# Kernel tuning notes

Measured on AMD Instinct MI355X. Metric: run time of the kernel, lower is better.

Reference implementation:

```python
import jax, jax.numpy as jnp
import numpy as np

N, E = 50000, 800000
NODE_IN, EDGE_IN, H, L = 2, 2, 128, 3
EPS = 1e-5


def _lin(x, W, b):
    return x @ W + b


def setup_inputs() -> dict:
    key = jax.random.key(0)
    ks = jax.random.split(key, 24)

    def gw(k, shape):
        fan_in = shape[-2]
        return jax.random.uniform(k, shape, jnp.float32, -1.0, 1.0) / np.sqrt(fan_in)

    inp = {
        "x": jax.random.normal(ks[0], (N, NODE_IN), jnp.float32),
        "edge_attr": jax.random.normal(ks[1], (E, EDGE_IN), jnp.float32),
        "edge_index": jax.random.randint(ks[2], (2, E), 0, N, jnp.int32),
        "batch": jnp.zeros((N,), jnp.int32),
        # input MLP: [NODE_IN -> H -> H], Lin+ReLU twice
        "Win0": gw(ks[3], (NODE_IN, H)), "bin0": jnp.zeros((H,), jnp.float32),
        "Win1": gw(ks[4], (H, H)), "bin1": jnp.zeros((H,), jnp.float32),
        # per-layer (stacked over L) IGConv params
        # mlp1: [H+EDGE_IN -> H -> H], Lin+ReLU twice
        "W1a": gw(ks[5], (L, H + EDGE_IN, H)), "b1a": jnp.zeros((L, H), jnp.float32),
        "W1b": gw(ks[6], (L, H, H)), "b1b": jnp.zeros((L, H), jnp.float32),
        # mlp2: [2H -> H] Lin+ReLU, then Lin+Sigmoid [H -> H]
        "W2a": gw(ks[7], (L, 2 * H, H)), "b2a": jnp.zeros((L, H), jnp.float32),
        "W2b": gw(ks[8], (L, H, H)), "b2b": jnp.zeros((L, H), jnp.float32),
        # BatchNorm affine params per layer
        "gamma": jnp.ones((L, H), jnp.float32), "beta": jnp.zeros((L, H), jnp.float32),
        # final MLP: [H -> H] Lin+ReLU, then Lin+Sigmoid [H -> 1]
        "Wf": gw(ks[9], (H, H)), "bf": jnp.zeros((H,), jnp.float32),
        "Wo": gw(ks[10], (H, 1)), "bo": jnp.zeros((1,), jnp.float32),
    }
    return inp


def _forward(x, edge_attr, edge_index, Win0, bin0, Win1, bin1,
             W1a, b1a, W1b, b1b, W2a, b2a, W2b, b2b, gamma, beta, Wf, bf, Wo, bo):
    src, dst = edge_index[0], edge_index[1]  # PyG source->target flow
    n = x.shape[0]

    # input MLP
    h = jax.nn.relu(_lin(x, Win0, bin0))
    h = jax.nn.relu(_lin(h, Win1, bin1))

    # per-edge mean-aggregation denominator (0-degree nodes -> 0 in PyG mean)
    cnt = jax.ops.segment_sum(jnp.ones((src.shape[0],), h.dtype), dst, num_segments=n)
    denom = jnp.maximum(cnt, 1.0)[:, None]  # [N,1]

    for l in range(L):
        # message: mlp1(cat(x_j, edge_attr))
        xj = h[src]                                        # [E,H] gather
        tmp = jnp.concatenate([xj, edge_attr], axis=1)     # [E,H+EDGE_IN]
        m = jax.nn.relu(_lin(tmp, W1a[l], b1a[l]))
        m = jax.nn.relu(_lin(m, W1b[l], b1b[l]))           # [E,H]
        # mean aggregate at targets
        agg = jax.ops.segment_sum(m, dst, num_segments=n) / denom  # [N,H]
        # update: mlp2(cat(x, agg)) -> Lin+ReLU -> Lin+Sigmoid
        u = jnp.concatenate([h, agg], axis=1)
        u = jax.nn.relu(_lin(u, W2a[l], b2a[l]))
        out = jax.nn.sigmoid(_lin(u, W2b[l], b2b[l]))
        # residual + BatchNorm (training-mode batch stats, biased var)
        r = h + out
        mu = jnp.mean(r, axis=0)
        var = jnp.mean((r - mu) ** 2, axis=0)
        h = (r - mu) * jax.lax.rsqrt(var + EPS) * gamma[l] + beta[l]

    # final MLP
    f = jax.nn.relu(_lin(h, Wf, bf))
    return jax.nn.sigmoid(_lin(f, Wo, bo))  # [N,1]


def reference(x, edge_attr, edge_index, batch, Win0, bin0, Win1, bin1,
              W1a, b1a, W1b, b1b, W2a, b2a, W2b, b2b, gamma, beta, Wf, bf, Wo, bo):
    # `batch` is unused by the original forward
    return _forward(x, edge_attr, edge_index, Win0, bin0, Win1, bin1,
                    W1a, b1a, W1b, b1b, W2a, b2a, W2b, b2b, gamma, beta,
                    Wf, bf, Wo, bo)
```

## Files before the change

### kernel.cpp

```cpp
#include <hip/hip_runtime.h>
#include <hip/hip_bf16.h>

#define NN 50000
#define NE 800000
#define HD 128
#define EPSV 1e-5f
#define TE 64
#define BLK 256
#define SROW 68
#define ASTR 336
#define BSTR 272

typedef unsigned short u16;
typedef __attribute__((ext_vector_type(8))) short bf16x8;
typedef __attribute__((ext_vector_type(4))) float f32x4;
#define MFMA16 __builtin_amdgcn_mfma_f32_16x16x32_bf16

__device__ __forceinline__ float sigm(float x){ return 1.0f/(1.0f+__expf(-x)); }
__device__ __forceinline__ void atomAddF(float* p, float v){ unsafeAtomicAdd(p, v); }
__device__ __forceinline__ unsigned bfr(float x){
    unsigned u = __float_as_uint(x);
    return (u + 0x7FFFu + ((u>>16)&1u)) >> 16;
}
__device__ __forceinline__ float bf2f(unsigned u){ return __uint_as_float(u<<16); }

__global__ void zero_i_k(int* __restrict__ p, int n){
    int i = blockIdx.x*blockDim.x + threadIdx.x;
    if (i < n) p[i] = 0;
}

__global__ void zero_agg_bn_k(float4* __restrict__ agg4, int n4, float* __restrict__ bn){
    int i = blockIdx.x*blockDim.x + threadIdx.x;
    if (i < n4) agg4[i] = make_float4(0.f,0.f,0.f,0.f);
    if (i < 256) bn[i] = 0.0f;
}

__global__ void count_k(const int* __restrict__ dst, int* __restrict__ cnt){
    int e = blockIdx.x*blockDim.x + threadIdx.x;
    if (e < NE) atomicAdd(&cnt[dst[e]], 1);
}
__global__ void rdenom_k(const int* __restrict__ cnt, float* __restrict__ rd){
    int i = blockIdx.x*blockDim.x + threadIdx.x;
    if (i < NN) rd[i] = 1.0f / fmaxf((float)cnt[i], 1.0f);
}

__global__ __launch_bounds__(1024) void scan_k(const int* __restrict__ cnt, int* __restrict__ off){
    __shared__ int s[1024];
    __shared__ int carryS;
    const int tid = threadIdx.x;
    if (tid == 0) carryS = 0;
    __syncthreads();
    const int NCH = (NN + 1023) / 1024;
    for (int ch = 0; ch < NCH; ++ch){
        const int i = ch*1024 + tid;
        const int v = (i < NN) ? cnt[i] : 0;
        s[tid] = v;
        __syncthreads();
        #pragma unroll
        for (int ofs = 1; ofs < 1024; ofs <<= 1){
            int t = (tid >= ofs) ? s[tid-ofs] : 0;
            __syncthreads();
            s[tid] += t;
            __syncthreads();
        }
        const int carry = carryS;
        if (i < NN) off[i] = carry + s[tid] - v;
        __syncthreads();
        if (tid == 1023) carryS = carry + s[1023];
        __syncthreads();
    }
    if (tid == 0) off[NN] = NE;
}

__global__ void fill_k(const int* __restrict__ src, const int* __restrict__ dst,
                       const float* __restrict__ ea, const int* __restrict__ off,
                       int* __restrict__ fill, int* __restrict__ ssrc,
                       unsigned* __restrict__ sea, int* __restrict__ sdst){
    int e = blockIdx.x*blockDim.x + threadIdx.x;
    if (e < NE){
        int d = dst[e];
        int pos = atomicAdd(&fill[d], 1);
        int slot = off[d] + pos;
        ssrc[slot] = src[e];
        sdst[slot] = d;
        const float2 a = *(const float2*)&ea[(size_t)e*2];
        sea[slot] = bfr(a.x) | (bfr(a.y)<<16);
    }
}

__global__ void wconv_k(const float* __restrict__ src, u16* __restrict__ dst,
                        int K, int KP, int H){
    int idx = blockIdx.x*blockDim.x + threadIdx.x;
    if (idx >= H*KP) return;
    const int l = blockIdx.y;
    src += (size_t)l*K*H;  dst += (size_t)l*H*KP;
    int c = idx / KP, k = idx - c*KP;
    dst[idx] = (k < K) ? (u16)bfr(src[k*H + c]) : (u16)0;
}

__device__ __forceinline__ void mv_acc(const float* sT, int krows,
        const float* __restrict__ W, int c0, int eg, float acc[4][8])
{
    const float* Wp = W + c0;
    #pragma unroll 2
    for (int k=0; k<krows; ++k) {
        const float4 sv = *(const float4*)(sT + k*SROW + eg*4);
        const float4 wa = *(const float4*)(Wp + k*HD);
        const float4 wb = *(const float4*)(Wp + k*HD + 4);
        const float s[4] = {sv.x, sv.y, sv.z, sv.w};
        const float w[8] = {wa.x,wa.y,wa.z,wa.w, wb.x,wb.y,wb.z,wb.w};
        #pragma unroll
        for (int i=0;i<4;++i)
            #pragma unroll
            for (int j=0;j<8;++j)
                acc[i][j] = fmaf(s[i], w[j], acc[i][j]);
    }
}

__device__ __forceinline__ void stage_rows(float* smem, const float* __restrict__ base,
                                           const int* rowsLDS, int tid)
{
    const int e_lo = tid>>3, kq = tid&7;
    #pragma unroll
    for (int half=0; half<2; ++half) {
        const int e = e_lo + 32*half;
        const int row = rowsLDS[e];
        const float* p = base + (size_t)row*HD + kq*4;
        #pragma unroll
        for (int q=0; q<4; ++q) {
            const float4 v = *(const float4*)(p + q*32);
            const int kb = 4*kq + 32*q;
            smem[(kb+0)*SROW + e] = v.x;
            smem[(kb+1)*SROW + e] = v.y;
            smem[(kb+2)*SROW + e] = v.z;
            smem[(kb+3)*SROW + e] = v.w;
        }
    }
}

__global__ __launch_bounds__(BLK) void input_mlp_k(
    const float* __restrict__ x,
    const float* __restrict__ W0, const float* __restrict__ b0,
    const float* __restrict__ W1, const float* __restrict__ b1,
    float* __restrict__ h, u16* __restrict__ hb)
{
    __shared__ float smem[130*SROW];
    const int tid = threadIdx.x;
    const int n0 = blockIdx.x * TE;

    #pragma unroll
    for (int it=0; it<(HD*TE)/BLK; ++it) {
        int task = it*BLK + tid;
        int e = task & (TE-1);
        int c = task >> 6;
        int n = n0 + e; if (n >= NN) n = NN-1;
        float x0 = x[n*2+0], x1 = x[n*2+1];
        smem[c*SROW + e] = fmaxf(fmaf(x0, W0[c], fmaf(x1, W0[HD+c], b0[c])), 0.0f);
    }
    __syncthreads();

    const int cg = tid & 15, eg = tid >> 4, c0 = cg*8;
    float acc[4][8];
    #pragma unroll
    for (int j=0;j<8;++j){ float bv=b1[c0+j];
        #pragma unroll
        for (int i=0;i<4;++i) acc[i][j]=bv; }
    mv_acc(smem, HD, W1, c0, eg, acc);

    #pragma unroll
    for (int i=0;i<4;++i){
        int n = n0 + eg*4 + i;
        if (n < NN) {
            float4 r0, r1;
            r0.x=fmaxf(acc[i][0],0.f); r0.y=fmaxf(acc[i][1],0.f);
            r0.z=fmaxf(acc[i][2],0.f); r0.w=fmaxf(acc[i][3],0.f);
            r1.x=fmaxf(acc[i][4],0.f); r1.y=fmaxf(acc[i][5],0.f);
            r1.z=fmaxf(acc[i][6],0.f); r1.w=fmaxf(acc[i][7],0.f);
            *(float4*)&h[(size_t)n*HD + c0]     = r0;
            *(float4*)&h[(size_t)n*HD + c0 + 4] = r1;
            uint4 pk;
            pk.x = bfr(r0.x)|(bfr(r0.y)<<16); pk.y = bfr(r0.z)|(bfr(r0.w)<<16);
            pk.z = bfr(r1.x)|(bfr(r1.y)<<16); pk.w = bfr(r1.z)|(bfr(r1.w)<<16);
            *(uint4*)&hb[(size_t)n*HD + c0] = pk;
        }
    }
}

__global__ __launch_bounds__(BLK, 7) void edge_msg_kernel(
    const u16* __restrict__ hb,
    const int* __restrict__ ssrc, const unsigned* __restrict__ sea,
    const int* __restrict__ sdst, const int* __restrict__ off,
    const float* __restrict__ rd,
    const u16* __restrict__ W1aT, const float* __restrict__ b1a,
    const u16* __restrict__ W1bT, const float* __restrict__ b1b,
    float* __restrict__ agg)
{
    __shared__ char bufA[TE*ASTR];

    const int tid = threadIdx.x;
    const int lane = tid & 63;
    const int l15 = lane & 15, lhi = lane >> 4;
    const int w = tid >> 6;
    const int s0 = blockIdx.x * TE;
    const int cg = tid & 15, c0 = cg*8;
    const int myrow = tid >> 2, p = tid & 3;
    const int rowL = 16*w + l15;
    const int bl = lane >> 2;

    const int d0 = sdst[s0];
    const int d1 = sdst[s0 + TE - 1];

    for (int idx = tid; idx < TE*4; idx += BLK){
        const int r = idx >> 2, q = idx & 3;
        *(uint4*)(bufA + r*ASTR + 272 + q*16) = make_uint4(0u,0u,0u,0u);
    }

    {
        const int sv0 = ssrc[s0 + rowL];
        const int sv  = __shfl(sv0, bl);
        const uint4* sp = (const uint4*)(hb + (size_t)sv*HD);
        uint4* dp = (uint4*)(bufA + myrow*ASTR + p*64);
        #pragma unroll
        for (int q=0;q<4;++q) dp[q] = sp[p*4+q];
        if (p == 0){
            const unsigned eaw = sea[s0 + myrow];
            *(uint4*)(bufA + myrow*ASTR + 256) = make_uint4(eaw, 0u, 0u, 0u);
        }
    }
    __syncthreads();

    f32x4 acc1[2][4];
    #pragma unroll
    for (int cc=0; cc<2; ++cc){
        const float4 bv = *(const float4*)&b1a[(2*w+cc)*16 + lhi*4];
        #pragma unroll
        for (int te=0; te<4; ++te){
            acc1[cc][te][0]=bv.x; acc1[cc][te][1]=bv.y;
            acc1[cc][te][2]=bv.z; acc1[cc][te][3]=bv.w;
        }
    }
    #pragma unroll
    for (int kk=0; kk<5; ++kk){
        const bf16x8 a0 = *(const bf16x8*)(W1aT + ((2*w  )*16 + l15)*160 + kk*32 + lhi*8);
        const bf16x8 a1 = *(const bf16x8*)(W1aT + ((2*w+1)*16 + l15)*160 + kk*32 + lhi*8);
        #pragma unroll
        for (int te=0; te<4; ++te){
            const bf16x8 bb = *(const bf16x8*)(bufA + (te*16+l15)*ASTR + kk*64 + lhi*16);
            acc1[0][te] = MFMA16(a0, bb, acc1[0][te], 0,0,0);
            acc1[1][te] = MFMA16(a1, bb, acc1[1][te], 0,0,0);
        }
    }
    __syncthreads();
    #pragma unroll
    for (int cc=0; cc<2; ++cc){
        #pragma unroll
        for (int te=0; te<4; ++te){
            uint2 pk;
            pk.x = bfr(fmaxf(acc1[cc][te][0],0.f)) | (bfr(fmaxf(acc1[cc][te][1],0.f))<<16);
            pk.y = bfr(fmaxf(acc1[cc][te][2],0.f)) | (bfr(fmaxf(acc1[cc][te][3],0.f))<<16);
            *(uint2*)(bufA + (te*16+l15)*ASTR + (2*w+cc)*32 + lhi*8) = pk;
        }
    }
    __syncthreads();

    f32x4 acc2[2][4];
    #pragma unroll
    for (int cc=0; cc<2; ++cc){
        const float4 bv = *(const float4*)&b1b[(2*w+cc)*16 + lhi*4];
        #pragma unroll
        for (int te=0; te<4; ++te){
            acc2[cc][te][0]=bv.x; acc2[cc][te][1]=bv.y;
            acc2[cc][te][2]=bv.z; acc2[cc][te][3]=bv.w;
        }
    }
    #pragma unroll
    for (int kk=0; kk<4; ++kk){
        const bf16x8 a0 = *(const bf16x8*)(W1bT + ((2*w  )*16 + l15)*128 + kk*32 + lhi*8);
        const bf16x8 a1 = *(const bf16x8*)(W1bT + ((2*w+1)*16 + l15)*128 + kk*32 + lhi*8);
        #pragma unroll
        for (int te=0; te<4; ++te){
            const bf16x8 bb = *(const bf16x8*)(bufA + (te*16+l15)*ASTR + kk*64 + lhi*16);
            acc2[0][te] = MFMA16(a0, bb, acc2[0][te], 0,0,0);
            acc2[1][te] = MFMA16(a1, bb, acc2[1][te], 0,0,0);
        }
    }
    __syncthreads();
    #pragma unroll
    for (int cc=0; cc<2; ++cc){
        #pragma unroll
        for (int te=0; te<4; ++te){
            uint2 pk;
            pk.x = bfr(fmaxf(acc2[cc][te][0],0.f)) | (bfr(fmaxf(acc2[cc][te][1],0.f))<<16);
            pk.y = bfr(fmaxf(acc2[cc][te][2],0.f)) | (bfr(fmaxf(acc2[cc][te][3],0.f))<<16);
            *(uint2*)(bufA + (te*16+l15)*ASTR + (2*w+cc)*32 + lhi*8) = pk;
        }
    }
    __syncthreads();

    const int ng = tid >> 4;
    for (int d = d0 + ng; d <= d1; d += 16){
        const int ob = off[d], oe = off[d+1];
        int lo = ob > s0 ? ob : s0;
        int hi = oe < s0 + TE ? oe : s0 + TE;
        if (lo >= hi) continue;
        float s[8] = {0.f,0.f,0.f,0.f,0.f,0.f,0.f,0.f};
        for (int t = lo; t < hi; ++t){
            const uint4 v = *(const uint4*)(bufA + (t - s0)*ASTR + cg*16);
            s[0] += bf2f(v.x&0xffffu); s[1] += bf2f(v.x>>16);
            s[2] += bf2f(v.y&0xffffu); s[3] += bf2f(v.y>>16);
            s[4] += bf2f(v.z&0xffffu); s[5] += bf2f(v.z>>16);
            s[6] += bf2f(v.w&0xffffu); s[7] += bf2f(v.w>>16);
        }
        const float rdv = rd[d];
        #pragma unroll
        for (int j=0;j<8;++j) s[j] *= rdv;
        float* ap = &agg[(size_t)d*HD + c0];
        if (ob >= s0 && oe <= s0 + TE){
            float4 a0 = make_float4(s[0],s[1],s[2],s[3]);
            float4 a1 = make_float4(s[4],s[5],s[6],s[7]);
            *(float4*)ap = a0; *(float4*)(ap+4) = a1;
        } else {
            #pragma unroll
            for (int j=0;j<8;++j) atomAddF(ap+j, s[j]);
        }
    }
}

__global__ __launch_bounds__(BLK, 4) void node_upd_kernel(
    const float* __restrict__ h, const u16* __restrict__ hb,
    const float* __restrict__ agg,
    const u16* __restrict__ W2aT, const float* __restrict__ b2a,
    const u16* __restrict__ W2bT, const float* __restrict__ b2b,
    float* __restrict__ rbuf)
{
    __shared__ char bufA[TE*ASTR];
    __shared__ char bufB[TE*BSTR];

    const int tid = threadIdx.x;
    const int lane = tid & 63;
    const int l15 = lane & 15, lhi = lane >> 4;
    const int w = tid >> 6;
    const int n0 = blockIdx.x * TE;
    const int myrow = tid >> 2, p = tid & 3;

    {
        int n = n0 + myrow; if (n >= NN) n = NN-1;
        const uint4* sp = (const uint4*)(hb + (size_t)n*HD);
        uint4* dp = (uint4*)(bufA + myrow*ASTR + p*64);
        #pragma unroll
        for (int q=0;q<4;++q) dp[q] = sp[p*4+q];
    }
    __syncthreads();

    f32x4 accN[2][4];
    #pragma unroll
    for (int cc=0; cc<2; ++cc){
        const float4 bv = *(const float4*)&b2a[(2*w+cc)*16 + lhi*4];
        #pragma unroll
        for (int te=0; te<4; ++te){
            accN[cc][te][0]=bv.x; accN[cc][te][1]=bv.y;
            accN[cc][te][2]=bv.z; accN[cc][te][3]=bv.w;
        }
    }
    #pragma unroll
    for (int kk=0; kk<4; ++kk){
        const bf16x8 a0 = *(const bf16x8*)(W2aT + ((2*w  )*16 + l15)*256 + kk*32 + lhi*8);
        const bf16x8 a1 = *(const bf16x8*)(W2aT + ((2*w+1)*16 + l15)*256 + kk*32 + lhi*8);
        #pragma unroll
        for (int te=0; te<4; ++te){
            const bf16x8 bb = *(const bf16x8*)(bufA + (te*16+l15)*ASTR + kk*64 + lhi*16);
            accN[0][te] = MFMA16(a0, bb, accN[0][te], 0,0,0);
            accN[1][te] = MFMA16(a1, bb, accN[1][te], 0,0,0);
        }
    }
    __syncthreads();
    {
        int n = n0 + myrow; if (n >= NN) n = NN-1;
        const float4* sp = (const float4*)(agg + (size_t)n*HD + p*32);
        uint4* dp = (uint4*)(bufA + myrow*ASTR + p*64);
        #pragma unroll
        for (int q=0;q<4;++q){
            const float4 v0 = sp[q*2+0], v1 = sp[q*2+1];
            uint4 pk;
            pk.x = bfr(v0.x)|(bfr(v0.y)<<16); pk.y = bfr(v0.z)|(bfr(v0.w)<<16);
            pk.z = bfr(v1.x)|(bfr(v1.y)<<16); pk.w = bfr(v1.z)|(bfr(v1.w)<<16);
            dp[q] = pk;
        }
    }
    __syncthreads();
    #pragma unroll
    for (int kk=0; kk<4; ++kk){
        const bf16x8 a0 = *(const bf16x8*)(W2aT + ((2*w  )*16 + l15)*256 + 128 + kk*32 + lhi*8);
        const bf16x8 a1 = *(const bf16x8*)(W2aT + ((2*w+1)*16 + l15)*256 + 128 + kk*32 + lhi*8);
        #pragma unroll
        for (int te=0; te<4; ++te){
            const bf16x8 bb = *(const bf16x8*)(bufA + (te*16+l15)*ASTR + kk*64 + lhi*16);
            accN[0][te] = MFMA16(a0, bb, accN[0][te], 0,0,0);
            accN[1][te] = MFMA16(a1, bb, accN[1][te], 0,0,0);
        }
    }
    #pragma unroll
    for (int cc=0; cc<2; ++cc){
        #pragma unroll
        for (int te=0; te<4; ++te){
            uint2 pk;
            pk.x = bfr(fmaxf(accN[cc][te][0],0.f)) | (bfr(fmaxf(accN[cc][te][1],0.f))<<16);
            pk.y = bfr(fmaxf(accN[cc][te][2],0.f)) | (bfr(fmaxf(accN[cc][te][3],0.f))<<16);
            *(uint2*)(bufB + (te*16+l15)*BSTR + (2*w+cc)*32 + lhi*8) = pk;
        }
    }
    __syncthreads();

    f32x4 accO[2][4];
    #pragma unroll
    for (int cc=0; cc<2; ++cc){
        const float4 bv = *(const float4*)&b2b[(2*w+cc)*16 + lhi*4];
        #pragma unroll
        for (int te=0; te<4; ++te){
            accO[cc][te][0]=bv.x; accO[cc][te][1]=bv.y;
            accO[cc][te][2]=bv.z; accO[cc][te][3]=bv.w;
        }
    }
    #pragma unroll
    for (int kk=0; kk<4; ++kk){
        const bf16x8 a0 = *(const bf16x8*)(W2bT + ((2*w  )*16 + l15)*128 + kk*32 + lhi*8);
        const bf16x8 a1 = *(const bf16x8*)(W2bT + ((2*w+1)*16 + l15)*128 + kk*32 + lhi*8);
        #pragma unroll
        for (int te=0; te<4; ++te){
            const bf16x8 bb = *(const bf16x8*)(bufB + (te*16+l15)*BSTR + kk*64 + lhi*16);
            accO[0][te] = MFMA16(a0, bb, accO[0][te], 0,0,0);
            accO[1][te] = MFMA16(a1, bb, accO[1][te], 0,0,0);
        }
    }
    #pragma unroll
    for (int cc=0; cc<2; ++cc){
        const int cbase = (2*w+cc)*16 + lhi*4;
        #pragma unroll
        for (int te=0; te<4; ++te){
            const int n = n0 + te*16 + l15;
            if (n < NN){
                const float4 hv = *(const float4*)&h[(size_t)n*HD + cbase];
                float4 r;
                r.x = hv.x + sigm(accO[cc][te][0]);
                r.y = hv.y + sigm(accO[cc][te][1]);
                r.z = hv.z + sigm(accO[cc][te][2]);
                r.w = hv.w + sigm(accO[cc][te][3]);
                *(float4*)&rbuf[(size_t)n*HD + cbase] = r;
            }
        }
    }
}

__global__ void bn_stats_k(const float* __restrict__ r, float* __restrict__ bn){
    const int c = threadIdx.x & (HD-1);
    const int half = threadIdx.x >> 7;
    const int stride = gridDim.x * 2;
    float s = 0.f, ss = 0.f;
    for (int n = blockIdx.x*2 + half; n < NN; n += stride) {
        const float v = r[(size_t)n*HD + c];
        s += v; ss += v*v;
    }
    atomAddF(&bn[c], s);
    atomAddF(&bn[HD+c], ss);
}

__global__ void bn_norm_k(const float* __restrict__ r, const float* __restrict__ bn,
                          const float* __restrict__ gamma, const float* __restrict__ beta,
                          float* __restrict__ h, u16* __restrict__ hb){
    const int i = blockIdx.x*blockDim.x + threadIdx.x;
    const int n4 = NN*HD/4;
    if (i >= n4) return;
    const int c0 = (i*4) & (HD-1);
    float4 v = ((const float4*)r)[i];
    float* vp = (float*)&v;
    #pragma unroll
    for (int j=0;j<4;++j){
        const int c = c0 + j;
        const float mu  = bn[c] * (1.0f/NN);
        const float var = bn[HD+c] * (1.0f/NN) - mu*mu;
        const float sc  = rsqrtf(var + EPSV) * gamma[c];
        const float sh  = beta[c] - mu*sc;
        vp[j] = fmaf(vp[j], sc, sh);
    }
    ((float4*)h)[i] = v;
    uint2 pk;
    pk.x = bfr(vp[0]) | (bfr(vp[1])<<16);
    pk.y = bfr(vp[2]) | (bfr(vp[3])<<16);
    ((uint2*)hb)[i] = pk;
}

__global__ __launch_bounds__(BLK) void final_kernel(
    const float* __restrict__ h,
    const float* __restrict__ Wf, const float* __restrict__ bf,
    const float* __restrict__ Wo, const float* __restrict__ bo,
    float* __restrict__ out)
{
    __shared__ float smem[130*SROW];
    __shared__ int s_src[TE];
    const int tid = threadIdx.x;
    const int n0 = blockIdx.x * TE;
    const int cg = tid & 15, eg = tid >> 4, c0 = cg*8;

    if (tid < TE) { int n = n0 + tid; s_src[tid] = (n < NN) ? n : NN-1; }
    __syncthreads();
    stage_rows(smem, h, s_src, tid);
    __syncthreads();

    float acc[4][8];
    #pragma unroll
    for (int j=0;j<8;++j){ float bv=bf[c0+j];
        #pragma unroll
        for (int i=0;i<4;++i) acc[i][j]=bv; }
    mv_acc(smem, HD, Wf, c0, eg, acc);
    __syncthreads();

    #pragma unroll
    for (int j=0;j<8;++j){
        float4 m0;
        m0.x=fmaxf(acc[0][j],0.f); m0.y=fmaxf(acc[1][j],0.f);
        m0.z=fmaxf(acc[2][j],0.f); m0.w=fmaxf(acc[3][j],0.f);
        *(float4*)&smem[(c0+j)*SROW + eg*4] = m0;
    }
    __syncthreads();

    const int e = tid >> 2, q = tid & 3;
    float s = 0.f;
    #pragma unroll
    for (int kk=0; kk<32; ++kk) {
        const int k = q*32 + kk;
        s = fmaf(smem[k*SROW + e], Wo[k], s);
    }
    s += __shfl_xor(s, 1);
    s += __shfl_xor(s, 2);
    const int n = n0 + e;
    if (q == 0 && n < NN)
        out[n] = sigm(s + bo[0]);
}

extern "C" void kernel_launch(void* const* d_in, const int* in_sizes, int n_in,
                              void* d_out, int out_size, void* d_ws, size_t ws_size,
                              hipStream_t stream)
{
    const float* x    = (const float*)d_in[0];
    const float* ea   = (const float*)d_in[1];
    const int*   ei   = (const int*)d_in[2];
    const float* Win0 = (const float*)d_in[4];
    const float* bin0 = (const float*)d_in[5];
    const float* Win1 = (const float*)d_in[6];
    const float* bin1 = (const float*)d_in[7];
    const float* W1a  = (const float*)d_in[8];
    const float* b1a  = (const float*)d_in[9];
    const float* W1b  = (const float*)d_in[10];
    const float* b1b  = (const float*)d_in[11];
    const float* W2a  = (const float*)d_in[12];
    const float* b2a  = (const float*)d_in[13];
    const float* W2b  = (const float*)d_in[14];
    const float* b2b  = (const float*)d_in[15];
    const float* gmm  = (const float*)d_in[16];
    const float* bta  = (const float*)d_in[17];
    const float* Wf   = (const float*)d_in[18];
    const float* bfv  = (const float*)d_in[19];
    const float* Wo   = (const float*)d_in[20];
    const float* bo   = (const float*)d_in[21];
    float* out = (float*)d_out;

    char* p = (char*)d_ws;
    float* h     = (float*)p;  p += (size_t)NN*HD*4;
    float* rbuf  = (float*)p;  p += (size_t)NN*HD*4;
    float* agg   = (float*)p;  p += (size_t)NN*HD*4;
    u16*   hb    = (u16*)p;    p += (size_t)NN*HD*2;
    u16*   W1aT  = (u16*)p;    p += (size_t)3*128*160*2;
    u16*   W1bT  = (u16*)p;    p += (size_t)3*128*128*2;
    u16*   W2aT  = (u16*)p;    p += (size_t)3*128*256*2;
    u16*   W2bT  = (u16*)p;    p += (size_t)3*128*128*2;
    float* rd    = (float*)p;  p += (size_t)NN*4;
    float* bn    = (float*)p;  p += 256*4;
    int*   cnt   = (int*)p;    p += (size_t)NN*4;
    int*   fill  = (int*)p;    p += (size_t)NN*4;
    int*   off   = (int*)p;    p += (size_t)(NN+1)*4;
    int*   ssrc  = (int*)p;    p += (size_t)NE*4;
    int*   sdst  = (int*)p;    p += (size_t)NE*4;
    unsigned* sea = (unsigned*)p;

    const int* srcp = ei;
    const int* dstp = ei + NE;

    const int GN = (NN + TE - 1) / TE;
    const int GE = NE / TE;
    const int G4 = (NN*HD/4 + 255) / 256;

    zero_i_k<<<(2*NN+255)/256, 256, 0, stream>>>(cnt, 2*NN);
    count_k<<<(NE+255)/256, 256, 0, stream>>>(dstp, cnt);
    scan_k<<<1, 1024, 0, stream>>>(cnt, off);
    rdenom_k<<<(NN+255)/256, 256, 0, stream>>>(cnt, rd);
    fill_k<<<(NE+255)/256, 256, 0, stream>>>(srcp, dstp, ea, off, fill, ssrc, sea, sdst);

    wconv_k<<<dim3((128*160+255)/256,3), 256, 0, stream>>>(W1a, W1aT, 130, 160, 128);
    wconv_k<<<dim3((128*128+255)/256,3), 256, 0, stream>>>(W1b, W1bT, 128, 128, 128);
    wconv_k<<<dim3((128*256+255)/256,3), 256, 0, stream>>>(W2a, W2aT, 256, 256, 128);
    wconv_k<<<dim3((128*128+255)/256,3), 256, 0, stream>>>(W2b, W2bT, 128, 128, 128);

    input_mlp_k<<<GN, BLK, 0, stream>>>(x, Win0, bin0, Win1, bin1, h, hb);

    for (int l = 0; l < 3; ++l) {
        zero_agg_bn_k<<<G4, 256, 0, stream>>>((float4*)agg, NN*HD/4, bn);
        edge_msg_kernel<<<GE, BLK, 0, stream>>>(hb, ssrc, sea, sdst, off, rd,
            W1aT + (size_t)l*128*160, b1a + l*HD,
            W1bT + (size_t)l*128*128, b1b + l*HD, agg);
        node_upd_kernel<<<GN, BLK, 0, stream>>>(h, hb, agg,
            W2aT + (size_t)l*128*256, b2a + l*HD,
            W2bT + (size_t)l*128*128, b2b + l*HD, rbuf);
        bn_stats_k<<<400, 256, 0, stream>>>(rbuf, bn);
        bn_norm_k<<<G4, 256, 0, stream>>>(rbuf, bn, gmm + l*HD, bta + l*HD, h, hb);
    }

    final_kernel<<<GN, BLK, 0, stream>>>(h, Wf, bfv, Wo, bo, out);
}
```

Baseline: 1.048 ms.

## Fuse BN stats into node update, parallelize scan, fold agg zeroing into BN

Replaces the single-block serial prefix scan with a three-kernel parallel block scan. Computes BatchNorm sum and sum-of-squares inside the node update epilogue with wave shuffles and atomics, which removes a separate full read of rbuf per layer. Zeroing of the aggregation buffer moves into the BN normalize kernel, and per-layer BN accumulators live in separate slots so they are zeroed once up front. This removes several launches and full-size memory passes, at the cost of more atomics and more stores in the normalize kernel.

```diff
diff --git a/kernel.cpp b/kernel.cpp
--- a/kernel.cpp
+++ b/kernel.cpp
@@ -32,7 +32,7 @@
 __global__ void zero_agg_bn_k(float4* __restrict__ agg4, int n4, float* __restrict__ bn){
     int i = blockIdx.x*blockDim.x + threadIdx.x;
     if (i < n4) agg4[i] = make_float4(0.f,0.f,0.f,0.f);
-    if (i < 256) bn[i] = 0.0f;
+    if (i < 768) bn[i] = 0.0f;
 }
 
 __global__ void count_k(const int* __restrict__ dst, int* __restrict__ cnt){
@@ -44,32 +44,36 @@
     if (i < NN) rd[i] = 1.0f / fmaxf((float)cnt[i], 1.0f);
 }
 
-__global__ __launch_bounds__(1024) void scan_k(const int* __restrict__ cnt, int* __restrict__ off){
-    __shared__ int s[1024];
-    __shared__ int carryS;
+__global__ __launch_bounds__(256) void scanA_k(const int* __restrict__ cnt,
+                                               int* __restrict__ off, int* __restrict__ bsum){
+    __shared__ int s[256];
+    const int b = blockIdx.x, tid = threadIdx.x, i = b*256 + tid;
+    const int v = (i < NN) ? cnt[i] : 0;
+    s[tid] = v; __syncthreads();
+    #pragma unroll
+    for (int ofs=1; ofs<256; ofs<<=1){
+        int t = (tid>=ofs) ? s[tid-ofs] : 0; __syncthreads();
+        s[tid] += t; __syncthreads();
+    }
+    if (i < NN) off[i] = s[tid] - v;
+    if (tid == 255) bsum[b] = s[255];
+}
+__global__ __launch_bounds__(256) void scanB_k(int* __restrict__ bsum, int nb){
+    __shared__ int s[256];
     const int tid = threadIdx.x;
-    if (tid == 0) carryS = 0;
-    __syncthreads();
-    const int NCH = (NN + 1023) / 1024;
-    for (int ch = 0; ch < NCH; ++ch){
-        const int i = ch*1024 + tid;
-        const int v = (i < NN) ? cnt[i] : 0;
-        s[tid] = v;
-        __syncthreads();
-        #pragma unroll
-        for (int ofs = 1; ofs < 1024; ofs <<= 1){
-            int t = (tid >= ofs) ? s[tid-ofs] : 0;
-            __syncthreads();
-            s[tid] += t;
-            __syncthreads();
-        }
-        const int carry = carryS;
-        if (i < NN) off[i] = carry + s[tid] - v;
-        __syncthreads();
-        if (tid == 1023) carryS = carry + s[1023];
-        __syncthreads();
-    }
-    if (tid == 0) off[NN] = NE;
+    const int v = (tid < nb) ? bsum[tid] : 0;
+    s[tid] = v; __syncthreads();
+    #pragma unroll
+    for (int ofs=1; ofs<256; ofs<<=1){
+        int t = (tid>=ofs) ? s[tid-ofs] : 0; __syncthreads();
+        s[tid] += t; __syncthreads();
+    }
+    if (tid < nb) bsum[tid] = s[tid] - v;
+}
+__global__ void scanC_k(int* __restrict__ off, const int* __restrict__ bsum){
+    const int b = blockIdx.x, i = b*256 + threadIdx.x;
+    if (i < NN) off[i] += bsum[b];
+    if (i == 0) off[NN] = NE;
 }
 
 __global__ void fill_k(const int* __restrict__ src, const int* __restrict__ dst,
@@ -331,7 +335,7 @@
     const float* __restrict__ agg,
     const u16* __restrict__ W2aT, const float* __restrict__ b2a,
     const u16* __restrict__ W2bT, const float* __restrict__ b2b,
-    float* __restrict__ rbuf)
+    float* __restrict__ rbuf, float* __restrict__ bn)
 {
     __shared__ char bufA[TE*ASTR];
     __shared__ char bufB[TE*BSTR];
@@ -432,6 +436,9 @@
             accO[1][te] = MFMA16(a1, bb, accO[1][te], 0,0,0);
         }
     }
+
+    float s1[2][4] = {{0.f,0.f,0.f,0.f},{0.f,0.f,0.f,0.f}};
+    float s2[2][4] = {{0.f,0.f,0.f,0.f},{0.f,0.f,0.f,0.f}};
     #pragma unroll
     for (int cc=0; cc<2; ++cc){
         const int cbase = (2*w+cc)*16 + lhi*4;
@@ -446,27 +453,31 @@
                 r.z = hv.z + sigm(accO[cc][te][2]);
                 r.w = hv.w + sigm(accO[cc][te][3]);
                 *(float4*)&rbuf[(size_t)n*HD + cbase] = r;
+                s1[cc][0]+=r.x; s1[cc][1]+=r.y; s1[cc][2]+=r.z; s1[cc][3]+=r.w;
+                s2[cc][0]+=r.x*r.x; s2[cc][1]+=r.y*r.y; s2[cc][2]+=r.z*r.z; s2[cc][3]+=r.w*r.w;
             }
         }
     }
-}
-
-__global__ void bn_stats_k(const float* __restrict__ r, float* __restrict__ bn){
-    const int c = threadIdx.x & (HD-1);
-    const int half = threadIdx.x >> 7;
-    const int stride = gridDim.x * 2;
-    float s = 0.f, ss = 0.f;
-    for (int n = blockIdx.x*2 + half; n < NN; n += stride) {
-        const float v = r[(size_t)n*HD + c];
-        s += v; ss += v*v;
-    }
-    atomAddF(&bn[c], s);
-    atomAddF(&bn[HD+c], ss);
+    #pragma unroll
+    for (int cc=0; cc<2; ++cc){
+        #pragma unroll
+        for (int j=0; j<4; ++j){
+            float a = s1[cc][j], b = s2[cc][j];
+            a += __shfl_xor(a,1); a += __shfl_xor(a,2); a += __shfl_xor(a,4); a += __shfl_xor(a,8);
+            b += __shfl_xor(b,1); b += __shfl_xor(b,2); b += __shfl_xor(b,4); b += __shfl_xor(b,8);
+            if (l15 == 0){
+                const int ch = (2*w+cc)*16 + lhi*4 + j;
+                atomAddF(&bn[ch], a);
+                atomAddF(&bn[HD+ch], b);
+            }
+        }
+    }
 }
 
 __global__ void bn_norm_k(const float* __restrict__ r, const float* __restrict__ bn,
                           const float* __restrict__ gamma, const float* __restrict__ beta,
-                          float* __restrict__ h, u16* __restrict__ hb){
+                          float* __restrict__ h, u16* __restrict__ hb,
+                          float4* __restrict__ agg4){
     const int i = blockIdx.x*blockDim.x + threadIdx.x;
     const int n4 = NN*HD/4;
     if (i >= n4) return;
@@ -487,6 +498,7 @@
     pk.x = bfr(vp[0]) | (bfr(vp[1])<<16);
     pk.y = bfr(vp[2]) | (bfr(vp[3])<<16);
     ((uint2*)hb)[i] = pk;
+    agg4[i] = make_float4(0.f,0.f,0.f,0.f);
 }
 
 __global__ __launch_bounds__(BLK) void final_kernel(
@@ -574,10 +586,11 @@
     u16*   W2aT  = (u16*)p;    p += (size_t)3*128*256*2;
     u16*   W2bT  = (u16*)p;    p += (size_t)3*128*128*2;
     float* rd    = (float*)p;  p += (size_t)NN*4;
-    float* bn    = (float*)p;  p += 256*4;
+    float* bn    = (float*)p;  p += 768*4;
     int*   cnt   = (int*)p;    p += (size_t)NN*4;
     int*   fill  = (int*)p;    p += (size_t)NN*4;
     int*   off   = (int*)p;    p += (size_t)(NN+1)*4;
+    int*   bsum  = (int*)p;    p += 256*4;
     int*   ssrc  = (int*)p;    p += (size_t)NE*4;
     int*   sdst  = (int*)p;    p += (size_t)NE*4;
     unsigned* sea = (unsigned*)p;
@@ -588,10 +601,13 @@
     const int GN = (NN + TE - 1) / TE;
     const int GE = NE / TE;
     const int G4 = (NN*HD/4 + 255) / 256;
+    const int NB = (NN + 255) / 256;
 
     zero_i_k<<<(2*NN+255)/256, 256, 0, stream>>>(cnt, 2*NN);
     count_k<<<(NE+255)/256, 256, 0, stream>>>(dstp, cnt);
-    scan_k<<<1, 1024, 0, stream>>>(cnt, off);
+    scanA_k<<<NB, 256, 0, stream>>>(cnt, off, bsum);
+    scanB_k<<<1, 256, 0, stream>>>(bsum, NB);
+    scanC_k<<<NB, 256, 0, stream>>>(off, bsum);
     rdenom_k<<<(NN+255)/256, 256, 0, stream>>>(cnt, rd);
     fill_k<<<(NE+255)/256, 256, 0, stream>>>(srcp, dstp, ea, off, fill, ssrc, sea, sdst);
 
@@ -600,18 +616,18 @@
     wconv_k<<<dim3((128*256+255)/256,3), 256, 0, stream>>>(W2a, W2aT, 256, 256, 128);
     wconv_k<<<dim3((128*128+255)/256,3), 256, 0, stream>>>(W2b, W2bT, 128, 128, 128);
 
+    zero_agg_bn_k<<<G4, 256, 0, stream>>>((float4*)agg, NN*HD/4, bn);
     input_mlp_k<<<GN, BLK, 0, stream>>>(x, Win0, bin0, Win1, bin1, h, hb);
 
     for (int l = 0; l < 3; ++l) {
-        zero_agg_bn_k<<<G4, 256, 0, stream>>>((float4*)agg, NN*HD/4, bn);
         edge_msg_kernel<<<GE, BLK, 0, stream>>>(hb, ssrc, sea, sdst, off, rd,
             W1aT + (size_t)l*128*160, b1a + l*HD,
             W1bT + (size_t)l*128*128, b1b + l*HD, agg);
         node_upd_kernel<<<GN, BLK, 0, stream>>>(h, hb, agg,
             W2aT + (size_t)l*128*256, b2a + l*HD,
-            W2bT + (size_t)l*128*128, b2b + l*HD, rbuf);
-        bn_stats_k<<<400, 256, 0, stream>>>(rbuf, bn);
-        bn_norm_k<<<G4, 256, 0, stream>>>(rbuf, bn, gmm + l*HD, bta + l*HD, h, hb);
+            W2bT + (size_t)l*128*128, b2b + l*HD, rbuf, bn + l*256);
+        bn_norm_k<<<G4, 256, 0, stream>>>(rbuf, bn + l*256, gmm + l*HD, bta + l*HD,
+                                          h, hb, (float4*)agg);
     }
 
     final_kernel<<<GN, BLK, 0, stream>>>(h, Wf, bfv, Wo, bo, out);
```

Result: slower. 1.076 ms (+2.7%).
